# Kernel tuning notes

Measured on AMD Instinct MI355X. Metric: run time of the kernel, lower is better.

## Reference

```python
import jax, jax.numpy as jnp
import numpy as np

N_NODES = 100000
N_EDGES = 1600000
IN_DIM = 64
HID = 32
OUT_DIM = 40


def setup_inputs() -> dict:
    key = jax.random.key(0)
    ks = jax.random.split(key, 9)
    x = jax.random.normal(ks[0], (N_NODES, IN_DIM), dtype=jnp.float32)
    edge_index = jax.random.randint(ks[1], (2, N_EDGES), 0, N_NODES, dtype=jnp.int64)
    # Xavier-ish scaled params (PyG SAGEConv: lin_l with bias, lin_r without)
    def glorot(k, shape):
        lim = float(np.sqrt(6.0 / (shape[0] + shape[1])))
        return jax.random.uniform(k, shape, jnp.float32, -lim, lim)
    W1l = glorot(ks[2], (IN_DIM, HID))
    b1 = jnp.zeros((HID,), jnp.float32)
    W1r = glorot(ks[3], (IN_DIM, HID))
    W2l = glorot(ks[4], (HID, HID))
    b2 = jnp.zeros((HID,), jnp.float32)
    W2r = glorot(ks[5], (HID, HID))
    w = glorot(ks[6], (HID, OUT_DIM))
    return {"x": x, "edge_index": edge_index, "W1l": W1l, "b1": b1,
            "W1r": W1r, "W2l": W2l, "b2": b2, "W2r": W2r, "w": w}


def reference(x, edge_index, W1l, b1, W1r, W2l, b2, W2r, w):
    src = edge_index[0]
    dst = edge_index[1]
    n = x.shape[0]
    # in-degree (for mean aggregation), clamp to avoid div-by-zero
    deg = jax.ops.segment_sum(jnp.ones((src.shape[0],), x.dtype), dst,
                              num_segments=n)
    inv_deg = 1.0 / jnp.maximum(deg, 1.0)  # [N]

    def sage_conv(h, Wl, b, Wr):
        # gather source features, scatter-mean to destinations
        agg = jax.ops.segment_sum(h[src], dst, num_segments=n)  # [N, d]
        agg = agg * inv_deg[:, None]
        return agg @ Wl + b + h @ Wr

    h = jax.nn.relu(sage_conv(x, W1l, b1, W1r))
    h = jax.nn.relu(sage_conv(h, W2l, b2, W2r))
    return h @ w
```

## Files before the change

### kernel.cpp

```cpp
#include <hip/hip_runtime.h>
#include <hip/hip_bf16.h>

#define N_NODES 100000
#define N_EDGES 1600000
#define IN_DIM 64
#define HID 32
#define OUT_DIM 40

#define NBUK 98
#define BCAP 18000
#define BIN_TILE 8192

__device__ __forceinline__ float bf2f(unsigned short u) {
    return __uint_as_float(((unsigned int)u) << 16);
}
__device__ __forceinline__ unsigned short f2bf(float f) {
    unsigned int u = __float_as_uint(f);
    u = (u + 0x7fffu + ((u >> 16) & 1u)) >> 16;
    return (unsigned short)u;
}

__global__ void detect_i64(const int* __restrict__ p, int* __restrict__ flagp) {
    __shared__ int s_any;
    if (threadIdx.x == 0) s_any = 0;
    __syncthreads();
    int any = 0;
    for (int i = threadIdx.x; i < 2048; i += blockDim.x) any |= p[2 * i + 1];
    if (any) atomicOr(&s_any, 1);
    __syncthreads();
    if (threadIdx.x == 0) *flagp = (s_any == 0) ? 1 : 0;
}

__device__ __forceinline__ int load_idx(const void* ei, int i64, long long pos) {
    if (i64) return (int)((const long long*)ei)[pos];
    return ((const int*)ei)[pos];
}

__global__ __launch_bounds__(1024) void bin_kernel(const void* __restrict__ ei,
                                                   const int* __restrict__ flagp,
                                                   int* __restrict__ cnt,
                                                   int* __restrict__ binned) {
    __shared__ int lcount[NBUK];
    __shared__ int lscan[NBUK + 1];
    __shared__ int lcur[NBUK];
    __shared__ int lbase[NBUK];
    __shared__ int stage[BIN_TILE];
    const int t = threadIdx.x;
    for (int i = t; i < NBUK; i += 1024) lcount[i] = 0;
    __syncthreads();

    const long long e0 = (long long)blockIdx.x * BIN_TILE;
    const int i64 = *flagp;
    int vv[8], bb[8];
#pragma unroll
    for (int k = 0; k < 8; ++k) {
        const long long e = e0 + (long long)k * 1024 + t;
        if (e < N_EDGES) {
            const int s = load_idx(ei, i64, e);
            const int d = load_idx(ei, i64, N_EDGES + e);
            bb[k] = d >> 10;
            vv[k] = (s << 10) | (d & 1023);
            atomicAdd(&lcount[bb[k]], 1);
        } else {
            bb[k] = -1;
        }
    }
    __syncthreads();
    if (t == 0) {
        int acc = 0;
        for (int i = 0; i < NBUK; ++i) {
            lscan[i] = acc;
            acc += lcount[i];
        }
        lscan[NBUK] = acc;
    }
    __syncthreads();
    for (int i = t; i < NBUK; i += 1024) {
        const int c = lcount[i];
        lbase[i] = i * BCAP + (c > 0 ? atomicAdd(&cnt[i], c) : 0);
        lcur[i] = lscan[i];
    }
    __syncthreads();
#pragma unroll
    for (int k = 0; k < 8; ++k) {
        if (bb[k] >= 0) {
            const int pos = atomicAdd(&lcur[bb[k]], 1);
            stage[pos] = vv[k];
        }
    }
    __syncthreads();
    const int total = lscan[NBUK];
    for (int j = t; j < total; j += 1024) {
        int lo = 0, hi = NBUK;
        while (hi - lo > 1) {
            const int mid = (lo + hi) >> 1;
            if (lscan[mid] <= j) lo = mid;
            else hi = mid;
        }
        binned[lbase[lo] + (j - lscan[lo])] = stage[j];
    }
}

__global__ __launch_bounds__(128) void bscan_kernel(const int* __restrict__ cnt,
                                                    int* __restrict__ bbase,
                                                    int* __restrict__ rowstart) {
    __shared__ int s[128];
    const int t = threadIdx.x;
    const int v = (t < NBUK) ? cnt[t] : 0;
    s[t] = v;
    __syncthreads();
    for (int off = 1; off < 128; off <<= 1) {
        const int add = (t >= off) ? s[t - off] : 0;
        __syncthreads();
        s[t] += add;
        __syncthreads();
    }
    if (t < NBUK) bbase[t] = s[t] - v;
    if (t == 0) rowstart[N_NODES] = N_EDGES;
}

__global__ __launch_bounds__(1024) void sort_kernel(const int* __restrict__ cnt,
                                                    const int* __restrict__ bbase,
                                                    const int* __restrict__ binned,
                                                    int* __restrict__ rowstart,
                                                    int* __restrict__ csr) {
    __shared__ int counts[1024];
    __shared__ int sc[1024];
    const int b = blockIdx.x;
    const int t = threadIdx.x;
    const int n = cnt[b];
    const int base = bbase[b];
    const int* __restrict__ bin = binned + (long long)b * BCAP;
    counts[t] = 0;
    __syncthreads();
    for (int i = t; i < n; i += 1024) atomicAdd(&counts[bin[i] & 1023], 1);
    __syncthreads();
    const int v = counts[t];
    sc[t] = v;
    __syncthreads();
    for (int off = 1; off < 1024; off <<= 1) {
        const int add = (t >= off) ? sc[t - off] : 0;
        __syncthreads();
        sc[t] += add;
        __syncthreads();
    }
    const int excl = sc[t] - v;
    const int node = b * 1024 + t;
    if (node < N_NODES) rowstart[node] = base + excl;
    counts[t] = excl;
    __syncthreads();
    for (int i = t; i < n; i += 1024) {
        const int vv = bin[i];
        const int pos = atomicAdd(&counts[vv & 1023], 1);
        csr[base + pos] = vv >> 10;
    }
}

__global__ __launch_bounds__(256) void lin1_kernel(
    const float* __restrict__ x, const float* __restrict__ Wl,
    const float* __restrict__ Wr, unsigned short* __restrict__ yl,
    float* __restrict__ yr) {
    __shared__ float sWl[IN_DIM * HID];
    __shared__ float sWr[IN_DIM * HID];
    __shared__ float sX[64 * IN_DIM];
    const int t = threadIdx.x;
    for (int i = t; i < IN_DIM * HID; i += 256) {
        sWl[i] = Wl[i];
        sWr[i] = Wr[i];
    }
    const long long r0 = (long long)blockIdx.x * 64;
    const int nrows = (int)((N_NODES - r0) < 64 ? (N_NODES - r0) : 64);
    const float4* xv = (const float4*)(x + r0 * IN_DIM);
    float4* sXv = (float4*)sX;
    for (int i = t; i < nrows * 16; i += 256) sXv[i] = xv[i];
    __syncthreads();

    const int c = t & 31;
    const int rbase = (t >> 5) * 8;
    float al[8] = {0, 0, 0, 0, 0, 0, 0, 0};
    float ar[8] = {0, 0, 0, 0, 0, 0, 0, 0};
    for (int k = 0; k < IN_DIM; k += 4) {
        const float wl0 = sWl[(k + 0) * HID + c];
        const float wl1 = sWl[(k + 1) * HID + c];
        const float wl2 = sWl[(k + 2) * HID + c];
        const float wl3 = sWl[(k + 3) * HID + c];
        const float wr0 = sWr[(k + 0) * HID + c];
        const float wr1 = sWr[(k + 1) * HID + c];
        const float wr2 = sWr[(k + 2) * HID + c];
        const float wr3 = sWr[(k + 3) * HID + c];
#pragma unroll
        for (int r = 0; r < 8; ++r) {
            const float4 xv4 = *(const float4*)&sX[(rbase + r) * IN_DIM + k];
            al[r] = fmaf(xv4.x, wl0, al[r]);
            al[r] = fmaf(xv4.y, wl1, al[r]);
            al[r] = fmaf(xv4.z, wl2, al[r]);
            al[r] = fmaf(xv4.w, wl3, al[r]);
            ar[r] = fmaf(xv4.x, wr0, ar[r]);
            ar[r] = fmaf(xv4.y, wr1, ar[r]);
            ar[r] = fmaf(xv4.z, wr2, ar[r]);
            ar[r] = fmaf(xv4.w, wr3, ar[r]);
        }
    }
#pragma unroll
    for (int r = 0; r < 8; ++r) {
        if (rbase + r < nrows) yr[(r0 + rbase + r) * HID + c] = ar[r];
    }
    __syncthreads();
    unsigned short* sB = (unsigned short*)sX;
#pragma unroll
    for (int r = 0; r < 8; ++r) {
        if (rbase + r < nrows) sB[(rbase + r) * HID + c] = f2bf(al[r]);
    }
    __syncthreads();
    uint4* dst = (uint4*)(yl + r0 * HID);
    const uint4* src = (const uint4*)sB;
    for (int i = t; i < nrows * 4; i += 256) dst[i] = src[i];
}

__global__ __launch_bounds__(256) void gather_lin2(
    const int* __restrict__ rowstart, const int* __restrict__ csr,
    const unsigned short* __restrict__ yl, const float* __restrict__ yr,
    const float* __restrict__ b, const float* __restrict__ W2l,
    const float* __restrict__ W2r, unsigned short* __restrict__ y2l,
    float* __restrict__ y2r) {
    __shared__ float sH[32 * 33];
    __shared__ float sW2l[HID * HID];
    __shared__ float sW2r[HID * HID];
    const int t = threadIdx.x;
    for (int i = t; i < HID * HID; i += 256) {
        sW2l[i] = W2l[i];
        sW2r[i] = W2r[i];
    }
    const int ln = t >> 3;
    const int q = t & 7;
    const int node = blockIdx.x * 32 + ln;
    const int start = rowstart[node];
    const int end = rowstart[node + 1];
    float ax = 0.f, ay = 0.f, az = 0.f, aw = 0.f;
    int e = start;
    for (; e + 1 < end; e += 2) {
        const int s0 = csr[e];
        const int s1 = csr[e + 1];
        const ushort4 v0 = *(const ushort4*)(yl + (long long)s0 * HID + q * 4);
        const ushort4 v1 = *(const ushort4*)(yl + (long long)s1 * HID + q * 4);
        ax += bf2f(v0.x) + bf2f(v1.x);
        ay += bf2f(v0.y) + bf2f(v1.y);
        az += bf2f(v0.z) + bf2f(v1.z);
        aw += bf2f(v0.w) + bf2f(v1.w);
    }
    if (e < end) {
        const int s0 = csr[e];
        const ushort4 v0 = *(const ushort4*)(yl + (long long)s0 * HID + q * 4);
        ax += bf2f(v0.x);
        ay += bf2f(v0.y);
        az += bf2f(v0.z);
        aw += bf2f(v0.w);
    }
    const float inv = 1.0f / fmaxf((float)(end - start), 1.0f);
    const float4 rr = *(const float4*)(yr + (long long)node * HID + q * 4);
    const float4 bb = *(const float4*)(b + q * 4);
    sH[ln * 33 + q * 4 + 0] = fmaxf(fmaf(ax, inv, bb.x) + rr.x, 0.f);
    sH[ln * 33 + q * 4 + 1] = fmaxf(fmaf(ay, inv, bb.y) + rr.y, 0.f);
    sH[ln * 33 + q * 4 + 2] = fmaxf(fmaf(az, inv, bb.z) + rr.z, 0.f);
    sH[ln * 33 + q * 4 + 3] = fmaxf(fmaf(aw, inv, bb.w) + rr.w, 0.f);
    __syncthreads();
    float l0 = 0, l1 = 0, l2 = 0, l3 = 0, m0 = 0, m1 = 0, m2 = 0, m3 = 0;
#pragma unroll
    for (int k = 0; k < HID; ++k) {
        const float hk = sH[ln * 33 + k];
        const float4 wl = *(const float4*)&sW2l[k * HID + q * 4];
        const float4 wr = *(const float4*)&sW2r[k * HID + q * 4];
        l0 = fmaf(hk, wl.x, l0);
        l1 = fmaf(hk, wl.y, l1);
        l2 = fmaf(hk, wl.z, l2);
        l3 = fmaf(hk, wl.w, l3);
        m0 = fmaf(hk, wr.x, m0);
        m1 = fmaf(hk, wr.y, m1);
        m2 = fmaf(hk, wr.z, m2);
        m3 = fmaf(hk, wr.w, m3);
    }
    *(float4*)(y2r + (long long)node * HID + q * 4) = make_float4(m0, m1, m2, m3);
    ushort4 p;
    p.x = f2bf(l0);
    p.y = f2bf(l1);
    p.z = f2bf(l2);
    p.w = f2bf(l3);
    *(ushort4*)(y2l + (long long)node * HID + q * 4) = p;
}

__global__ __launch_bounds__(256) void gather_out(
    const int* __restrict__ rowstart, const int* __restrict__ csr,
    const unsigned short* __restrict__ yl, const float* __restrict__ yr,
    const float* __restrict__ b, const float* __restrict__ w,
    float* __restrict__ out) {
    __shared__ float sH[32 * 33];
    __shared__ float sW[HID * OUT_DIM];
    const int t = threadIdx.x;
    for (int i = t; i < HID * OUT_DIM; i += 256) sW[i] = w[i];
    const int ln = t >> 3;
    const int q = t & 7;
    const int node = blockIdx.x * 32 + ln;
    const int start = rowstart[node];
    const int end = rowstart[node + 1];
    float ax = 0.f, ay = 0.f, az = 0.f, aw = 0.f;
    int e = start;
    for (; e + 1 < end; e += 2) {
        const int s0 = csr[e];
        const int s1 = csr[e + 1];
        const ushort4 v0 = *(const ushort4*)(yl + (long long)s0 * HID + q * 4);
        const ushort4 v1 = *(const ushort4*)(yl + (long long)s1 * HID + q * 4);
        ax += bf2f(v0.x) + bf2f(v1.x);
        ay += bf2f(v0.y) + bf2f(v1.y);
        az += bf2f(v0.z) + bf2f(v1.z);
        aw += bf2f(v0.w) + bf2f(v1.w);
    }
    if (e < end) {
        const int s0 = csr[e];
        const ushort4 v0 = *(const ushort4*)(yl + (long long)s0 * HID + q * 4);
        ax += bf2f(v0.x);
        ay += bf2f(v0.y);
        az += bf2f(v0.z);
        aw += bf2f(v0.w);
    }
    const float inv = 1.0f / fmaxf((float)(end - start), 1.0f);
    const float4 rr = *(const float4*)(yr + (long long)node * HID + q * 4);
    const float4 bb = *(const float4*)(b + q * 4);
    sH[ln * 33 + q * 4 + 0] = fmaxf(fmaf(ax, inv, bb.x) + rr.x, 0.f);
    sH[ln * 33 + q * 4 + 1] = fmaxf(fmaf(ay, inv, bb.y) + rr.y, 0.f);
    sH[ln * 33 + q * 4 + 2] = fmaxf(fmaf(az, inv, bb.z) + rr.z, 0.f);
    sH[ln * 33 + q * 4 + 3] = fmaxf(fmaf(aw, inv, bb.w) + rr.w, 0.f);
    __syncthreads();
    float acc[5] = {0, 0, 0, 0, 0};
#pragma unroll
    for (int k = 0; k < HID; ++k) {
        const float hk = sH[ln * 33 + k];
#pragma unroll
        for (int j = 0; j < 5; ++j)
            acc[j] = fmaf(hk, sW[k * OUT_DIM + q + 8 * j], acc[j]);
    }
#pragma unroll
    for (int j = 0; j < 5; ++j) out[(long long)node * OUT_DIM + q + 8 * j] = acc[j];
}

extern "C" void kernel_launch(void* const* d_in, const int* in_sizes, int n_in,
                              void* d_out, int out_size, void* d_ws,
                              size_t ws_size, hipStream_t stream) {
    const float* x = (const float*)d_in[0];
    const void* ei = d_in[1];
    const float* W1l = (const float*)d_in[2];
    const float* b1 = (const float*)d_in[3];
    const float* W1r = (const float*)d_in[4];
    const float* W2l = (const float*)d_in[5];
    const float* b2 = (const float*)d_in[6];
    const float* W2r = (const float*)d_in[7];
    const float* w = (const float*)d_in[8];
    float* out = (float*)d_out;

    int* ip = (int*)d_ws;
    int* flagp = ip;
    int* cnt = ip + 64;
    int* bbase = ip + 192;
    int* rowstart = ip + 320;
    int* csr = rowstart + 100032;
    float* Y1r = (float*)(csr + N_EDGES);
    float* Y2r = Y1r + (long long)N_NODES * HID;
    unsigned short* Y1l = (unsigned short*)(Y2r + (long long)N_NODES * HID);
    unsigned short* Y2l = Y1l + (long long)N_NODES * HID;
    int* binned = (int*)Y2r;

    hipMemsetAsync(cnt, 0, 128 * sizeof(int), stream);
    detect_i64<<<1, 256, 0, stream>>>((const int*)ei, flagp);

    bin_kernel<<<(N_EDGES + BIN_TILE - 1) / BIN_TILE, 1024, 0, stream>>>(
        ei, flagp, cnt, binned);
    bscan_kernel<<<1, 128, 0, stream>>>(cnt, bbase, rowstart);
    sort_kernel<<<NBUK, 1024, 0, stream>>>(cnt, bbase, binned, rowstart, csr);

    lin1_kernel<<<(N_NODES + 63) / 64, 256, 0, stream>>>(x, W1l, W1r, Y1l, Y1r);

    gather_lin2<<<N_NODES / 32, 256, 0, stream>>>(rowstart, csr, Y1l, Y1r, b1,
                                                  W2l, W2r, Y2l, Y2r);

    gather_out<<<N_NODES / 32, 256, 0, stream>>>(rowstart, csr, Y2l, Y2r, b2, w,
                                                 out);
}
```

Before: 152.0 us.

## Balance edge gather across block threads and double sort bucket count

The gather kernels no longer give each node 8 threads that walk its own edge list. Each block now spreads all edges of its 32 nodes evenly over 256 threads, locates the owning node by binary search over shared row starts, and accumulates into shared memory with atomics. This removes load imbalance from skewed degrees but adds shared-memory atomics and search overhead. Separately, CSR bucketing doubles to 196 buckets of 512 nodes so the sort kernel runs more, smaller blocks.

After: 400.3 us. 163% more time.

```diff
diff --git a/kernel.cpp b/kernel.cpp
--- a/kernel.cpp
+++ b/kernel.cpp
@@ -7,8 +7,8 @@
 #define HID 32
 #define OUT_DIM 40
 
-#define NBUK 98
-#define BCAP 18000
+#define NBUK 196
+#define BCAP 9216
 #define BIN_TILE 8192
 
 __device__ __forceinline__ float bf2f(unsigned short u) {
@@ -58,8 +58,8 @@
         if (e < N_EDGES) {
             const int s = load_idx(ei, i64, e);
             const int d = load_idx(ei, i64, N_EDGES + e);
-            bb[k] = d >> 10;
-            vv[k] = (s << 10) | (d & 1023);
+            bb[k] = d >> 9;
+            vv[k] = (s << 9) | (d & 511);
             atomicAdd(&lcount[bb[k]], 1);
         } else {
             bb[k] = -1;
@@ -101,15 +101,15 @@
     }
 }
 
-__global__ __launch_bounds__(128) void bscan_kernel(const int* __restrict__ cnt,
+__global__ __launch_bounds__(256) void bscan_kernel(const int* __restrict__ cnt,
                                                     int* __restrict__ bbase,
                                                     int* __restrict__ rowstart) {
-    __shared__ int s[128];
+    __shared__ int s[256];
     const int t = threadIdx.x;
     const int v = (t < NBUK) ? cnt[t] : 0;
     s[t] = v;
     __syncthreads();
-    for (int off = 1; off < 128; off <<= 1) {
+    for (int off = 1; off < 256; off <<= 1) {
         const int add = (t >= off) ? s[t - off] : 0;
         __syncthreads();
         s[t] += add;
@@ -119,13 +119,13 @@
     if (t == 0) rowstart[N_NODES] = N_EDGES;
 }
 
-__global__ __launch_bounds__(1024) void sort_kernel(const int* __restrict__ cnt,
-                                                    const int* __restrict__ bbase,
-                                                    const int* __restrict__ binned,
-                                                    int* __restrict__ rowstart,
-                                                    int* __restrict__ csr) {
-    __shared__ int counts[1024];
-    __shared__ int sc[1024];
+__global__ __launch_bounds__(512) void sort_kernel(const int* __restrict__ cnt,
+                                                   const int* __restrict__ bbase,
+                                                   const int* __restrict__ binned,
+                                                   int* __restrict__ rowstart,
+                                                   int* __restrict__ csr) {
+    __shared__ int counts[512];
+    __shared__ int sc[512];
     const int b = blockIdx.x;
     const int t = threadIdx.x;
     const int n = cnt[b];
@@ -133,26 +133,26 @@
     const int* __restrict__ bin = binned + (long long)b * BCAP;
     counts[t] = 0;
     __syncthreads();
-    for (int i = t; i < n; i += 1024) atomicAdd(&counts[bin[i] & 1023], 1);
+    for (int i = t; i < n; i += 512) atomicAdd(&counts[bin[i] & 511], 1);
     __syncthreads();
     const int v = counts[t];
     sc[t] = v;
     __syncthreads();
-    for (int off = 1; off < 1024; off <<= 1) {
+    for (int off = 1; off < 512; off <<= 1) {
         const int add = (t >= off) ? sc[t - off] : 0;
         __syncthreads();
         sc[t] += add;
         __syncthreads();
     }
     const int excl = sc[t] - v;
-    const int node = b * 1024 + t;
+    const int node = b * 512 + t;
     if (node < N_NODES) rowstart[node] = base + excl;
     counts[t] = excl;
     __syncthreads();
-    for (int i = t; i < n; i += 1024) {
+    for (int i = t; i < n; i += 512) {
         const int vv = bin[i];
-        const int pos = atomicAdd(&counts[vv & 1023], 1);
-        csr[base + pos] = vv >> 10;
+        const int pos = atomicAdd(&counts[vv & 511], 1);
+        csr[base + pos] = vv >> 9;
     }
 }
 
@@ -217,57 +217,115 @@
     for (int i = t; i < nrows * 4; i += 256) dst[i] = src[i];
 }
 
+__device__ __forceinline__ void edge_accum(const int* __restrict__ csr,
+                                           const unsigned short* __restrict__ yl,
+                                           const int* srow, float* acc, int t) {
+    const int q = t & 7;
+    const int estart = srow[0];
+    const int eend = srow[32];
+    const int nE = eend - estart;
+    const int nPair = (nE + 1) >> 1;
+    for (int i = t; i < nPair * 8; i += 256) {
+        const int e0 = estart + ((i >> 3) << 1);
+        const int e1 = e0 + 1;
+        const int s0 = csr[e0];
+        int lo = 0, hi = 32;
+#pragma unroll
+        for (int step = 0; step < 5; ++step) {
+            const int mid = (lo + hi) >> 1;
+            if (srow[mid] <= e0) lo = mid;
+            else hi = mid;
+        }
+        const ushort4 v0 = *(const ushort4*)(yl + (long long)s0 * HID + q * 4);
+        float fx = bf2f(v0.x), fy = bf2f(v0.y), fz = bf2f(v0.z), fw = bf2f(v0.w);
+        const bool has1 = (e1 < eend);
+        if (has1 && e1 < srow[lo + 1]) {
+            const int s1 = csr[e1];
+            const ushort4 v1 = *(const ushort4*)(yl + (long long)s1 * HID + q * 4);
+            fx += bf2f(v1.x);
+            fy += bf2f(v1.y);
+            fz += bf2f(v1.z);
+            fw += bf2f(v1.w);
+            float* a = &acc[lo * 33 + q * 4];
+            atomicAdd(a + 0, fx);
+            atomicAdd(a + 1, fy);
+            atomicAdd(a + 2, fz);
+            atomicAdd(a + 3, fw);
+        } else {
+            float* a = &acc[lo * 33 + q * 4];
+            atomicAdd(a + 0, fx);
+            atomicAdd(a + 1, fy);
+            atomicAdd(a + 2, fz);
+            atomicAdd(a + 3, fw);
+            if (has1) {
+                const int s1 = csr[e1];
+                const ushort4 v1 =
+                    *(const ushort4*)(yl + (long long)s1 * HID + q * 4);
+                int lo1 = 0, hi1 = 32;
+#pragma unroll
+                for (int step = 0; step < 5; ++step) {
+                    const int mid = (lo1 + hi1) >> 1;
+                    if (srow[mid] <= e1) lo1 = mid;
+                    else hi1 = mid;
+                }
+                float* a1 = &acc[lo1 * 33 + q * 4];
+                atomicAdd(a1 + 0, bf2f(v1.x));
+                atomicAdd(a1 + 1, bf2f(v1.y));
+                atomicAdd(a1 + 2, bf2f(v1.z));
+                atomicAdd(a1 + 3, bf2f(v1.w));
+            }
+        }
+    }
+}
+
 __global__ __launch_bounds__(256) void gather_lin2(
     const int* __restrict__ rowstart, const int* __restrict__ csr,
     const unsigned short* __restrict__ yl, const float* __restrict__ yr,
     const float* __restrict__ b, const float* __restrict__ W2l,
     const float* __restrict__ W2r, unsigned short* __restrict__ y2l,
     float* __restrict__ y2r) {
-    __shared__ float sH[32 * 33];
+    __shared__ float acc[32 * 33];
     __shared__ float sW2l[HID * HID];
     __shared__ float sW2r[HID * HID];
+    __shared__ int srow[33];
     const int t = threadIdx.x;
     for (int i = t; i < HID * HID; i += 256) {
         sW2l[i] = W2l[i];
         sW2r[i] = W2r[i];
     }
+    const int n0 = blockIdx.x * 32;
+    if (t < 33) srow[t] = rowstart[n0 + t];
+    for (int i = t; i < 32 * 33; i += 256) acc[i] = 0.f;
+    __syncthreads();
+
+    edge_accum(csr, yl, srow, acc, t);
+    __syncthreads();
+
     const int ln = t >> 3;
     const int q = t & 7;
-    const int node = blockIdx.x * 32 + ln;
-    const int start = rowstart[node];
-    const int end = rowstart[node + 1];
-    float ax = 0.f, ay = 0.f, az = 0.f, aw = 0.f;
-    int e = start;
-    for (; e + 1 < end; e += 2) {
-        const int s0 = csr[e];
-        const int s1 = csr[e + 1];
-        const ushort4 v0 = *(const ushort4*)(yl + (long long)s0 * HID + q * 4);
-        const ushort4 v1 = *(const ushort4*)(yl + (long long)s1 * HID + q * 4);
-        ax += bf2f(v0.x) + bf2f(v1.x);
-        ay += bf2f(v0.y) + bf2f(v1.y);
-        az += bf2f(v0.z) + bf2f(v1.z);
-        aw += bf2f(v0.w) + bf2f(v1.w);
-    }
-    if (e < end) {
-        const int s0 = csr[e];
-        const ushort4 v0 = *(const ushort4*)(yl + (long long)s0 * HID + q * 4);
-        ax += bf2f(v0.x);
-        ay += bf2f(v0.y);
-        az += bf2f(v0.z);
-        aw += bf2f(v0.w);
-    }
-    const float inv = 1.0f / fmaxf((float)(end - start), 1.0f);
+    const int node = n0 + ln;
+    const int deg = srow[ln + 1] - srow[ln];
+    const float inv = 1.0f / fmaxf((float)deg, 1.0f);
+    float a0 = acc[ln * 33 + q * 4 + 0];
+    float a1 = acc[ln * 33 + q * 4 + 1];
+    float a2 = acc[ln * 33 + q * 4 + 2];
+    float a3 = acc[ln * 33 + q * 4 + 3];
     const float4 rr = *(const float4*)(yr + (long long)node * HID + q * 4);
     const float4 bb = *(const float4*)(b + q * 4);
-    sH[ln * 33 + q * 4 + 0] = fmaxf(fmaf(ax, inv, bb.x) + rr.x, 0.f);
-    sH[ln * 33 + q * 4 + 1] = fmaxf(fmaf(ay, inv, bb.y) + rr.y, 0.f);
-    sH[ln * 33 + q * 4 + 2] = fmaxf(fmaf(az, inv, bb.z) + rr.z, 0.f);
-    sH[ln * 33 + q * 4 + 3] = fmaxf(fmaf(aw, inv, bb.w) + rr.w, 0.f);
+    a0 = fmaxf(fmaf(a0, inv, bb.x) + rr.x, 0.f);
+    a1 = fmaxf(fmaf(a1, inv, bb.y) + rr.y, 0.f);
+    a2 = fmaxf(fmaf(a2, inv, bb.z) + rr.z, 0.f);
+    a3 = fmaxf(fmaf(a3, inv, bb.w) + rr.w, 0.f);
+    __syncthreads();
+    acc[ln * 33 + q * 4 + 0] = a0;
+    acc[ln * 33 + q * 4 + 1] = a1;
+    acc[ln * 33 + q * 4 + 2] = a2;
+    acc[ln * 33 + q * 4 + 3] = a3;
     __syncthreads();
     float l0 = 0, l1 = 0, l2 = 0, l3 = 0, m0 = 0, m1 = 0, m2 = 0, m3 = 0;
 #pragma unroll
     for (int k = 0; k < HID; ++k) {
-        const float hk = sH[ln * 33 + k];
+        const float hk = acc[ln * 33 + k];
         const float4 wl = *(const float4*)&sW2l[k * HID + q * 4];
         const float4 wr = *(const float4*)&sW2r[k * HID + q * 4];
         l0 = fmaf(hk, wl.x, l0);
@@ -293,53 +351,50 @@
     const unsigned short* __restrict__ yl, const float* __restrict__ yr,
     const float* __restrict__ b, const float* __restrict__ w,
     float* __restrict__ out) {
-    __shared__ float sH[32 * 33];
+    __shared__ float acc[32 * 33];
     __shared__ float sW[HID * OUT_DIM];
+    __shared__ int srow[33];
     const int t = threadIdx.x;
     for (int i = t; i < HID * OUT_DIM; i += 256) sW[i] = w[i];
+    const int n0 = blockIdx.x * 32;
+    if (t < 33) srow[t] = rowstart[n0 + t];
+    for (int i = t; i < 32 * 33; i += 256) acc[i] = 0.f;
+    __syncthreads();
+
+    edge_accum(csr, yl, srow, acc, t);
+    __syncthreads();
+
     const int ln = t >> 3;
     const int q = t & 7;
-    const int node = blockIdx.x * 32 + ln;
-    const int start = rowstart[node];
-    const int end = rowstart[node + 1];
-    float ax = 0.f, ay = 0.f, az = 0.f, aw = 0.f;
-    int e = start;
-    for (; e + 1 < end; e += 2) {
-        const int s0 = csr[e];
-        const int s1 = csr[e + 1];
-        const ushort4 v0 = *(const ushort4*)(yl + (long long)s0 * HID + q * 4);
-        const ushort4 v1 = *(const ushort4*)(yl + (long long)s1 * HID + q * 4);
-        ax += bf2f(v0.x) + bf2f(v1.x);
-        ay += bf2f(v0.y) + bf2f(v1.y);
-        az += bf2f(v0.z) + bf2f(v1.z);
-        aw += bf2f(v0.w) + bf2f(v1.w);
-    }
-    if (e < end) {
-        const int s0 = csr[e];
-        const ushort4 v0 = *(const ushort4*)(yl + (long long)s0 * HID + q * 4);
-        ax += bf2f(v0.x);
-        ay += bf2f(v0.y);
-        az += bf2f(v0.z);
-        aw += bf2f(v0.w);
-    }
-    const float inv = 1.0f / fmaxf((float)(end - start), 1.0f);
+    const int node = n0 + ln;
+    const int deg = srow[ln + 1] - srow[ln];
+    const float inv = 1.0f / fmaxf((float)deg, 1.0f);
+    float a0 = acc[ln * 33 + q * 4 + 0];
+    float a1 = acc[ln * 33 + q * 4 + 1];
+    float a2 = acc[ln * 33 + q * 4 + 2];
+    float a3 = acc[ln * 33 + q * 4 + 3];
     const float4 rr = *(const float4*)(yr + (long long)node * HID + q * 4);
     const float4 bb = *(const float4*)(b + q * 4);
-    sH[ln * 33 + q * 4 + 0] = fmaxf(fmaf(ax, inv, bb.x) + rr.x, 0.f);
-    sH[ln * 33 + q * 4 + 1] = fmaxf(fmaf(ay, inv, bb.y) + rr.y, 0.f);
-    sH[ln * 33 + q * 4 + 2] = fmaxf(fmaf(az, inv, bb.z) + rr.z, 0.f);
-    sH[ln * 33 + q * 4 + 3] = fmaxf(fmaf(aw, inv, bb.w) + rr.w, 0.f);
-    __syncthreads();
-    float acc[5] = {0, 0, 0, 0, 0};
+    a0 = fmaxf(fmaf(a0, inv, bb.x) + rr.x, 0.f);
+    a1 = fmaxf(fmaf(a1, inv, bb.y) + rr.y, 0.f);
+    a2 = fmaxf(fmaf(a2, inv, bb.z) + rr.z, 0.f);
+    a3 = fmaxf(fmaf(a3, inv, bb.w) + rr.w, 0.f);
+    __syncthreads();
+    acc[ln * 33 + q * 4 + 0] = a0;
+    acc[ln * 33 + q * 4 + 1] = a1;
+    acc[ln * 33 + q * 4 + 2] = a2;
+    acc[ln * 33 + q * 4 + 3] = a3;
+    __syncthreads();
+    float o[5] = {0, 0, 0, 0, 0};
 #pragma unroll
     for (int k = 0; k < HID; ++k) {
-        const float hk = sH[ln * 33 + k];
+        const float hk = acc[ln * 33 + k];
 #pragma unroll
         for (int j = 0; j < 5; ++j)
-            acc[j] = fmaf(hk, sW[k * OUT_DIM + q + 8 * j], acc[j]);
-    }
-#pragma unroll
-    for (int j = 0; j < 5; ++j) out[(long long)node * OUT_DIM + q + 8 * j] = acc[j];
+            o[j] = fmaf(hk, sW[k * OUT_DIM + q + 8 * j], o[j]);
+    }
+#pragma unroll
+    for (int j = 0; j < 5; ++j) out[(long long)node * OUT_DIM + q + 8 * j] = o[j];
 }
 
 extern "C" void kernel_launch(void* const* d_in, const int* in_sizes, int n_in,
@@ -359,8 +414,8 @@
     int* ip = (int*)d_ws;
     int* flagp = ip;
     int* cnt = ip + 64;
-    int* bbase = ip + 192;
-    int* rowstart = ip + 320;
+    int* bbase = ip + 320;
+    int* rowstart = ip + 576;
     int* csr = rowstart + 100032;
     float* Y1r = (float*)(csr + N_EDGES);
     float* Y2r = Y1r + (long long)N_NODES * HID;
@@ -368,13 +423,13 @@
     unsigned short* Y2l = Y1l + (long long)N_NODES * HID;
     int* binned = (int*)Y2r;
 
-    hipMemsetAsync(cnt, 0, 128 * sizeof(int), stream);
+    hipMemsetAsync(cnt, 0, 256 * sizeof(int), stream);
     detect_i64<<<1, 256, 0, stream>>>((const int*)ei, flagp);
 
     bin_kernel<<<(N_EDGES + BIN_TILE - 1) / BIN_TILE, 1024, 0, stream>>>(
         ei, flagp, cnt, binned);
-    bscan_kernel<<<1, 128, 0, stream>>>(cnt, bbase, rowstart);
-    sort_kernel<<<NBUK, 1024, 0, stream>>>(cnt, bbase, binned, rowstart, csr);
+    bscan_kernel<<<1, 256, 0, stream>>>(cnt, bbase, rowstart);
+    sort_kernel<<<NBUK, 512, 0, stream>>>(cnt, bbase, binned, rowstart, csr);
 
     lin1_kernel<<<(N_NODES + 63) / 64, 256, 0, stream>>>(x, W1l, W1r, Y1l, Y1r);
 
```

## Split each node's gather across four edge slots and double sort buckets

Applied to the files above, without the earlier changes.

The gather kernels now assign 32 threads per node instead of 8. Four edge slots stride through the neighbor list and are combined with cross-lane shuffles, which exposes more memory-level parallelism per node and shortens the per-node dependency chains. Each block now handles 8 nodes, and the follow-on small matmuls are remapped so that one thread computes one output column. Separately, the CSR build uses 196 buckets of 512 nodes, giving the sort kernel more, smaller blocks. In exchange there are four times as many gather blocks, each reloading the weights into shared memory, plus extra shuffle work.

Measured after the change: 160.1 us. +5.3%, slower.

```diff
diff --git a/kernel.cpp b/kernel.cpp
--- a/kernel.cpp
+++ b/kernel.cpp
@@ -7,8 +7,8 @@
 #define HID 32
 #define OUT_DIM 40
 
-#define NBUK 98
-#define BCAP 18000
+#define NBUK 196
+#define BCAP 9216
 #define BIN_TILE 8192
 
 __device__ __forceinline__ float bf2f(unsigned short u) {
@@ -58,8 +58,8 @@
         if (e < N_EDGES) {
             const int s = load_idx(ei, i64, e);
             const int d = load_idx(ei, i64, N_EDGES + e);
-            bb[k] = d >> 10;
-            vv[k] = (s << 10) | (d & 1023);
+            bb[k] = d >> 9;
+            vv[k] = (s << 9) | (d & 511);
             atomicAdd(&lcount[bb[k]], 1);
         } else {
             bb[k] = -1;
@@ -101,15 +101,15 @@
     }
 }
 
-__global__ __launch_bounds__(128) void bscan_kernel(const int* __restrict__ cnt,
+__global__ __launch_bounds__(256) void bscan_kernel(const int* __restrict__ cnt,
                                                     int* __restrict__ bbase,
                                                     int* __restrict__ rowstart) {
-    __shared__ int s[128];
+    __shared__ int s[256];
     const int t = threadIdx.x;
     const int v = (t < NBUK) ? cnt[t] : 0;
     s[t] = v;
     __syncthreads();
-    for (int off = 1; off < 128; off <<= 1) {
+    for (int off = 1; off < 256; off <<= 1) {
         const int add = (t >= off) ? s[t - off] : 0;
         __syncthreads();
         s[t] += add;
@@ -119,13 +119,13 @@
     if (t == 0) rowstart[N_NODES] = N_EDGES;
 }
 
-__global__ __launch_bounds__(1024) void sort_kernel(const int* __restrict__ cnt,
-                                                    const int* __restrict__ bbase,
-                                                    const int* __restrict__ binned,
-                                                    int* __restrict__ rowstart,
-                                                    int* __restrict__ csr) {
-    __shared__ int counts[1024];
-    __shared__ int sc[1024];
+__global__ __launch_bounds__(512) void sort_kernel(const int* __restrict__ cnt,
+                                                   const int* __restrict__ bbase,
+                                                   const int* __restrict__ binned,
+                                                   int* __restrict__ rowstart,
+                                                   int* __restrict__ csr) {
+    __shared__ int counts[512];
+    __shared__ int sc[512];
     const int b = blockIdx.x;
     const int t = threadIdx.x;
     const int n = cnt[b];
@@ -133,26 +133,26 @@
     const int* __restrict__ bin = binned + (long long)b * BCAP;
     counts[t] = 0;
     __syncthreads();
-    for (int i = t; i < n; i += 1024) atomicAdd(&counts[bin[i] & 1023], 1);
+    for (int i = t; i < n; i += 512) atomicAdd(&counts[bin[i] & 511], 1);
     __syncthreads();
     const int v = counts[t];
     sc[t] = v;
     __syncthreads();
-    for (int off = 1; off < 1024; off <<= 1) {
+    for (int off = 1; off < 512; off <<= 1) {
         const int add = (t >= off) ? sc[t - off] : 0;
         __syncthreads();
         sc[t] += add;
         __syncthreads();
     }
     const int excl = sc[t] - v;
-    const int node = b * 1024 + t;
+    const int node = b * 512 + t;
     if (node < N_NODES) rowstart[node] = base + excl;
     counts[t] = excl;
     __syncthreads();
-    for (int i = t; i < n; i += 1024) {
+    for (int i = t; i < n; i += 512) {
         const int vv = bin[i];
-        const int pos = atomicAdd(&counts[vv & 1023], 1);
-        csr[base + pos] = vv >> 10;
+        const int pos = atomicAdd(&counts[vv & 511], 1);
+        csr[base + pos] = vv >> 9;
     }
 }
 
@@ -217,30 +217,15 @@
     for (int i = t; i < nrows * 4; i += 256) dst[i] = src[i];
 }
 
-__global__ __launch_bounds__(256) void gather_lin2(
-    const int* __restrict__ rowstart, const int* __restrict__ csr,
-    const unsigned short* __restrict__ yl, const float* __restrict__ yr,
-    const float* __restrict__ b, const float* __restrict__ W2l,
-    const float* __restrict__ W2r, unsigned short* __restrict__ y2l,
-    float* __restrict__ y2r) {
-    __shared__ float sH[32 * 33];
-    __shared__ float sW2l[HID * HID];
-    __shared__ float sW2r[HID * HID];
-    const int t = threadIdx.x;
-    for (int i = t; i < HID * HID; i += 256) {
-        sW2l[i] = W2l[i];
-        sW2r[i] = W2r[i];
-    }
-    const int ln = t >> 3;
-    const int q = t & 7;
-    const int node = blockIdx.x * 32 + ln;
-    const int start = rowstart[node];
-    const int end = rowstart[node + 1];
+__device__ __forceinline__ void gather_node32(
+    const int* __restrict__ csr, const unsigned short* __restrict__ yl,
+    const float* __restrict__ yr, const float* __restrict__ b, int node,
+    int start, int end, int slot, int q, float* sHrow) {
     float ax = 0.f, ay = 0.f, az = 0.f, aw = 0.f;
-    int e = start;
-    for (; e + 1 < end; e += 2) {
+    int e = start + slot;
+    for (; e + 4 < end; e += 8) {
         const int s0 = csr[e];
-        const int s1 = csr[e + 1];
+        const int s1 = csr[e + 4];
         const ushort4 v0 = *(const ushort4*)(yl + (long long)s0 * HID + q * 4);
         const ushort4 v1 = *(const ushort4*)(yl + (long long)s1 * HID + q * 4);
         ax += bf2f(v0.x) + bf2f(v1.x);
@@ -256,36 +241,62 @@
         az += bf2f(v0.z);
         aw += bf2f(v0.w);
     }
+    ax += __shfl_xor(ax, 8, 32);
+    ay += __shfl_xor(ay, 8, 32);
+    az += __shfl_xor(az, 8, 32);
+    aw += __shfl_xor(aw, 8, 32);
+    ax += __shfl_xor(ax, 16, 32);
+    ay += __shfl_xor(ay, 16, 32);
+    az += __shfl_xor(az, 16, 32);
+    aw += __shfl_xor(aw, 16, 32);
     const float inv = 1.0f / fmaxf((float)(end - start), 1.0f);
     const float4 rr = *(const float4*)(yr + (long long)node * HID + q * 4);
     const float4 bb = *(const float4*)(b + q * 4);
-    sH[ln * 33 + q * 4 + 0] = fmaxf(fmaf(ax, inv, bb.x) + rr.x, 0.f);
-    sH[ln * 33 + q * 4 + 1] = fmaxf(fmaf(ay, inv, bb.y) + rr.y, 0.f);
-    sH[ln * 33 + q * 4 + 2] = fmaxf(fmaf(az, inv, bb.z) + rr.z, 0.f);
-    sH[ln * 33 + q * 4 + 3] = fmaxf(fmaf(aw, inv, bb.w) + rr.w, 0.f);
-    __syncthreads();
-    float l0 = 0, l1 = 0, l2 = 0, l3 = 0, m0 = 0, m1 = 0, m2 = 0, m3 = 0;
+    if (slot == 0) {
+        sHrow[q * 4 + 0] = fmaxf(fmaf(ax, inv, bb.x) + rr.x, 0.f);
+        sHrow[q * 4 + 1] = fmaxf(fmaf(ay, inv, bb.y) + rr.y, 0.f);
+        sHrow[q * 4 + 2] = fmaxf(fmaf(az, inv, bb.z) + rr.z, 0.f);
+        sHrow[q * 4 + 3] = fmaxf(fmaf(aw, inv, bb.w) + rr.w, 0.f);
+    }
+}
+
+__global__ __launch_bounds__(256) void gather_lin2(
+    const int* __restrict__ rowstart, const int* __restrict__ csr,
+    const unsigned short* __restrict__ yl, const float* __restrict__ yr,
+    const float* __restrict__ b, const float* __restrict__ W2l,
+    const float* __restrict__ W2r, unsigned short* __restrict__ y2l,
+    float* __restrict__ y2r) {
+    __shared__ float sH[8 * 33];
+    __shared__ float sW2l[HID * HID];
+    __shared__ float sW2r[HID * HID];
+    __shared__ int srow[9];
+    const int t = threadIdx.x;
+    for (int i = t; i < HID * HID; i += 256) {
+        sW2l[i] = W2l[i];
+        sW2r[i] = W2r[i];
+    }
+    const int n0 = blockIdx.x * 8;
+    if (t < 9) srow[t] = rowstart[n0 + t];
+    __syncthreads();
+
+    const int g = t >> 5;
+    const int sub = t & 31;
+    const int slot = sub >> 3;
+    const int q = sub & 7;
+    const int node = n0 + g;
+    gather_node32(csr, yl, yr, b, node, srow[g], srow[g + 1], slot, q,
+                  &sH[g * 33]);
+    __syncthreads();
+
+    float l = 0.f, m = 0.f;
 #pragma unroll
     for (int k = 0; k < HID; ++k) {
-        const float hk = sH[ln * 33 + k];
-        const float4 wl = *(const float4*)&sW2l[k * HID + q * 4];
-        const float4 wr = *(const float4*)&sW2r[k * HID + q * 4];
-        l0 = fmaf(hk, wl.x, l0);
-        l1 = fmaf(hk, wl.y, l1);
-        l2 = fmaf(hk, wl.z, l2);
-        l3 = fmaf(hk, wl.w, l3);
-        m0 = fmaf(hk, wr.x, m0);
-        m1 = fmaf(hk, wr.y, m1);
-        m2 = fmaf(hk, wr.z, m2);
-        m3 = fmaf(hk, wr.w, m3);
-    }
-    *(float4*)(y2r + (long long)node * HID + q * 4) = make_float4(m0, m1, m2, m3);
-    ushort4 p;
-    p.x = f2bf(l0);
-    p.y = f2bf(l1);
-    p.z = f2bf(l2);
-    p.w = f2bf(l3);
-    *(ushort4*)(y2l + (long long)node * HID + q * 4) = p;
+        const float hk = sH[g * 33 + k];
+        l = fmaf(hk, sW2l[k * HID + sub], l);
+        m = fmaf(hk, sW2r[k * HID + sub], m);
+    }
+    y2r[(long long)node * HID + sub] = m;
+    y2l[(long long)node * HID + sub] = f2bf(l);
 }
 
 __global__ __launch_bounds__(256) void gather_out(
@@ -293,53 +304,33 @@
     const unsigned short* __restrict__ yl, const float* __restrict__ yr,
     const float* __restrict__ b, const float* __restrict__ w,
     float* __restrict__ out) {
-    __shared__ float sH[32 * 33];
+    __shared__ float sH[8 * 33];
     __shared__ float sW[HID * OUT_DIM];
+    __shared__ int srow[9];
     const int t = threadIdx.x;
     for (int i = t; i < HID * OUT_DIM; i += 256) sW[i] = w[i];
-    const int ln = t >> 3;
-    const int q = t & 7;
-    const int node = blockIdx.x * 32 + ln;
-    const int start = rowstart[node];
-    const int end = rowstart[node + 1];
-    float ax = 0.f, ay = 0.f, az = 0.f, aw = 0.f;
-    int e = start;
-    for (; e + 1 < end; e += 2) {
-        const int s0 = csr[e];
-        const int s1 = csr[e + 1];
-        const ushort4 v0 = *(const ushort4*)(yl + (long long)s0 * HID + q * 4);
-        const ushort4 v1 = *(const ushort4*)(yl + (long long)s1 * HID + q * 4);
-        ax += bf2f(v0.x) + bf2f(v1.x);
-        ay += bf2f(v0.y) + bf2f(v1.y);
-        az += bf2f(v0.z) + bf2f(v1.z);
-        aw += bf2f(v0.w) + bf2f(v1.w);
-    }
-    if (e < end) {
-        const int s0 = csr[e];
-        const ushort4 v0 = *(const ushort4*)(yl + (long long)s0 * HID + q * 4);
-        ax += bf2f(v0.x);
-        ay += bf2f(v0.y);
-        az += bf2f(v0.z);
-        aw += bf2f(v0.w);
-    }
-    const float inv = 1.0f / fmaxf((float)(end - start), 1.0f);
-    const float4 rr = *(const float4*)(yr + (long long)node * HID + q * 4);
-    const float4 bb = *(const float4*)(b + q * 4);
-    sH[ln * 33 + q * 4 + 0] = fmaxf(fmaf(ax, inv, bb.x) + rr.x, 0.f);
-    sH[ln * 33 + q * 4 + 1] = fmaxf(fmaf(ay, inv, bb.y) + rr.y, 0.f);
-    sH[ln * 33 + q * 4 + 2] = fmaxf(fmaf(az, inv, bb.z) + rr.z, 0.f);
-    sH[ln * 33 + q * 4 + 3] = fmaxf(fmaf(aw, inv, bb.w) + rr.w, 0.f);
-    __syncthreads();
-    float acc[5] = {0, 0, 0, 0, 0};
+    const int n0 = blockIdx.x * 8;
+    if (t < 9) srow[t] = rowstart[n0 + t];
+    __syncthreads();
+
+    const int g = t >> 5;
+    const int sub = t & 31;
+    const int slot = sub >> 3;
+    const int q = sub & 7;
+    const int node = n0 + g;
+    gather_node32(csr, yl, yr, b, node, srow[g], srow[g + 1], slot, q,
+                  &sH[g * 33]);
+    __syncthreads();
+
+    float o0 = 0.f, o1 = 0.f;
 #pragma unroll
     for (int k = 0; k < HID; ++k) {
-        const float hk = sH[ln * 33 + k];
-#pragma unroll
-        for (int j = 0; j < 5; ++j)
-            acc[j] = fmaf(hk, sW[k * OUT_DIM + q + 8 * j], acc[j]);
-    }
-#pragma unroll
-    for (int j = 0; j < 5; ++j) out[(long long)node * OUT_DIM + q + 8 * j] = acc[j];
+        const float hk = sH[g * 33 + k];
+        o0 = fmaf(hk, sW[k * OUT_DIM + sub], o0);
+        o1 = fmaf(hk, sW[k * OUT_DIM + 32 + (sub & 7)], o1);
+    }
+    out[(long long)node * OUT_DIM + sub] = o0;
+    if (sub < 8) out[(long long)node * OUT_DIM + 32 + sub] = o1;
 }
 
 extern "C" void kernel_launch(void* const* d_in, const int* in_sizes, int n_in,
@@ -359,8 +350,8 @@
     int* ip = (int*)d_ws;
     int* flagp = ip;
     int* cnt = ip + 64;
-    int* bbase = ip + 192;
-    int* rowstart = ip + 320;
+    int* bbase = ip + 320;
+    int* rowstart = ip + 576;
     int* csr = rowstart + 100032;
     float* Y1r = (float*)(csr + N_EDGES);
     float* Y2r = Y1r + (long long)N_NODES * HID;
@@ -368,19 +359,19 @@
     unsigned short* Y2l = Y1l + (long long)N_NODES * HID;
     int* binned = (int*)Y2r;
 
-    hipMemsetAsync(cnt, 0, 128 * sizeof(int), stream);
+    hipMemsetAsync(cnt, 0, 256 * sizeof(int), stream);
     detect_i64<<<1, 256, 0, stream>>>((const int*)ei, flagp);
 
     bin_kernel<<<(N_EDGES + BIN_TILE - 1) / BIN_TILE, 1024, 0, stream>>>(
         ei, flagp, cnt, binned);
-    bscan_kernel<<<1, 128, 0, stream>>>(cnt, bbase, rowstart);
-    sort_kernel<<<NBUK, 1024, 0, stream>>>(cnt, bbase, binned, rowstart, csr);
+    bscan_kernel<<<1, 256, 0, stream>>>(cnt, bbase, rowstart);
+    sort_kernel<<<NBUK, 512, 0, stream>>>(cnt, bbase, binned, rowstart, csr);
 
     lin1_kernel<<<(N_NODES + 63) / 64, 256, 0, stream>>>(x, W1l, W1r, Y1l, Y1r);
 
-    gather_lin2<<<N_NODES / 32, 256, 0, stream>>>(rowstart, csr, Y1l, Y1r, b1,
-                                                  W2l, W2r, Y2l, Y2r);
-
-    gather_out<<<N_NODES / 32, 256, 0, stream>>>(rowstart, csr, Y2l, Y2r, b2, w,
-                                                 out);
-}
+    gather_lin2<<<N_NODES / 8, 256, 0, stream>>>(rowstart, csr, Y1l, Y1r, b1,
+                                                 W2l, W2r, Y2l, Y2r);
+
+    gather_out<<<N_NODES / 8, 256, 0, stream>>>(rowstart, csr, Y2l, Y2r, b2, w,
+                                                out);
+}
```
